# Performance work log

Hardware: AMD Instinct MI355X
Metric: run time of the kernel (lower is better)

Reference implementation:

```python
import jax, jax.numpy as jnp
import numpy as np

B, F = 65536, 300
SIGMA = 2.0
ALPHA = 1.0


def _gaussian_kernel(sigma):
    l = int(np.round(3 * sigma + 1.0))  # 7 for sigma=2
    x = np.linspace(-(l - 1.0) / 2.0, (l - 1.0) / 2.0, l)
    k = np.exp(-0.5 * np.square(x) / np.square(sigma))
    return (k / k.sum()).astype(np.float32)


def setup_inputs() -> dict:
    key = jax.random.key(0)
    fr_funcs = jax.random.normal(key, (B, F), dtype=jnp.float32)
    freqs = np.arange(1, F + 1, dtype=np.float32)
    freqs = (freqs - freqs.min()) / (freqs.max() - freqs.min())
    freqs = freqs * 2.0 - 1.0  # normalized to [-1, 1], as in __init__
    return {
        "fr_funcs": fr_funcs,
        "freqs": jnp.asarray(freqs),
        "kernel": jnp.asarray(_gaussian_kernel(SIGMA)),
    }


def _first_peak_loss(f, freqs):
    # Replicates softlocalmax's first segment.
    # find_peaks on symmetric-padded signal => boundary is a peak iff it
    # strictly exceeds its single neighbor; interior peaks are strict local maxima.
    n = f.shape[0]
    interior = (f[1:-1] > f[:-2]) & (f[1:-1] > f[2:])
    is_peak = jnp.concatenate([f[0:1] > f[1:2], interior, f[-1:] > f[-2:-1]])
    idx = jnp.where(is_peak, jnp.arange(n, dtype=jnp.int32), n)
    two = jnp.sort(idx)[:2]  # first two peak positions (n if absent)
    npeaks = jnp.sum(is_peak.astype(jnp.int32))
    # first segment end: midpoint of first two peaks (int truncation), else n-1
    end = jnp.where(npeaks >= 2, (two[0] + two[1]) // 2, n - 1)
    mask = jnp.arange(n) < end
    logits = jnp.where(mask, f * ALPHA, -jnp.inf)
    w = jax.nn.softmax(logits)  # zeros outside segment == softmax over slice
    softargmax = w @ freqs
    return -softargmax


def reference(fr_funcs, freqs, kernel):
    # Gaussian1DBlur: conv1d with padding='same' (zero padding, odd kernel)
    blurred = jax.lax.conv_general_dilated(
        fr_funcs[:, None, :], kernel[None, None, :], (1,), "SAME"
    )[:, 0]  # (B, F)
    return jax.vmap(_first_peak_loss, in_axes=(0, None))(blurred, freqs)
```

## Files before the change

### kernel.cpp

```cpp
#include <hip/hip_runtime.h>
#include <math.h>

#define NF 300
#define NC 75
#define ROWS 32
#define G 8
#define CPL 10

#define CONV(b0,b1,b2,b3,c0,c1,c2,A,B) \
    b0 = kk[0]*c0;  b0=fmaf(kk[1],c1 ,b0); b0=fmaf(kk[2],c2 ,b0); b0=fmaf(kk[3],A.x,b0); b0=fmaf(kk[4],A.y,b0); b0=fmaf(kk[5],A.z,b0); b0=fmaf(kk[6],A.w,b0); \
    b1 = kk[0]*c1;  b1=fmaf(kk[1],c2 ,b1); b1=fmaf(kk[2],A.x,b1); b1=fmaf(kk[3],A.y,b1); b1=fmaf(kk[4],A.z,b1); b1=fmaf(kk[5],A.w,b1); b1=fmaf(kk[6],B.x,b1); \
    b2 = kk[0]*c2;  b2=fmaf(kk[1],A.x,b2); b2=fmaf(kk[2],A.y,b2); b2=fmaf(kk[3],A.z,b2); b2=fmaf(kk[4],A.w,b2); b2=fmaf(kk[5],B.x,b2); b2=fmaf(kk[6],B.y,b2); \
    b3 = kk[0]*A.x; b3=fmaf(kk[1],A.y,b3); b3=fmaf(kk[2],A.z,b3); b3=fmaf(kk[3],A.w,b3); b3=fmaf(kk[4],B.x,b3); b3=fmaf(kk[5],B.y,b3); b3=fmaf(kk[6],B.z,b3);

__global__ __launch_bounds__(256) void peak_mover_loss_kernel(
    const float* __restrict__ in,
    const float* __restrict__ freqs,
    const float* __restrict__ kw,
    float* __restrict__ out)
{
    __shared__ __align__(16) float lds[ROWS * NF];

    const int tid = threadIdx.x;
    const int rowBase = blockIdx.x * ROWS;

    {
        const float4* gin = reinterpret_cast<const float4*>(in + (size_t)rowBase * NF);
        float4* l4 = reinterpret_cast<float4*>(lds);
#pragma unroll
        for (int i = 0; i < 10; ++i) {
            const int idx = tid + 256 * i;
            if (idx < ROWS * NC) l4[idx] = gin[idx];
        }
    }

    float kk[7];
#pragma unroll
    for (int t = 0; t < 7; ++t) kk[t] = kw[t];

    __syncthreads();

    const int g = tid >> 3;
    const int l = tid & 7;
    const float4* rp4 = reinterpret_cast<const float4*>(lds + g * NF);

    const int cs = CPL * l;
    const int nc = (l == G - 1) ? (NC - cs) : CPL;

    float c0, c1, c2, prev1, prev2;
    if (l == 0) {
        c0 = c1 = c2 = 0.f; prev1 = prev2 = -INFINITY;
    } else {
        const float4 P = rp4[cs - 2];
        const float4 Q = rp4[cs - 1];
        const float4 Rv = rp4[cs];
        float pb0, pb1, pb2, pb3;
        float pc0 = P.y, pc1 = P.z, pc2 = P.w;
        CONV(pb0, pb1, pb2, pb3, pc0, pc1, pc2, Q, Rv);
        (void)pb0; (void)pb1;
        prev2 = pb2; prev1 = pb3;
        c0 = Q.y; c1 = Q.z; c2 = Q.w;
    }

    int cnt = 0, p0 = 0, p1 = 0;
    float4 A = rp4[cs];
    for (int t = 0; t < nc; ++t) {
        const int m = cs + t;
        float4 B = make_float4(0.f, 0.f, 0.f, 0.f);
        if (m + 1 < NC) B = rp4[m + 1];
        float b0, b1, b2, b3;
        CONV(b0, b1, b2, b3, c0, c1, c2, A, B);
        const int base = 4 * m;
        if (prev1 > prev2 && prev1 > b0) { if (cnt==0) p0=base-1; else if (cnt==1) p1=base-1; ++cnt; }
        if (b0 > prev1 && b0 > b1)       { if (cnt==0) p0=base;   else if (cnt==1) p1=base;   ++cnt; }
        if (b1 > b0 && b1 > b2)          { if (cnt==0) p0=base+1; else if (cnt==1) p1=base+1; ++cnt; }
        if (b2 > b1 && b2 > b3)          { if (cnt==0) p0=base+2; else if (cnt==1) p1=base+2; ++cnt; }
        prev2 = b2; prev1 = b3;
        c0 = A.y; c1 = A.z; c2 = A.w;
        A = B;
    }
    if (l == G - 1 && prev1 > prev2) { if (cnt==0) p0=NF-1; else if (cnt==1) p1=NF-1; ++cnt; }

#pragma unroll
    for (int o = 1; o < G; o <<= 1) {
        const int oc = __shfl_xor(cnt, o, G);
        const int q0 = __shfl_xor(p0, o, G);
        const int q1 = __shfl_xor(p1, o, G);
        const bool right = (l & o) != 0;
        const int Lc = right ? oc : cnt, Rc = right ? cnt : oc;
        const int L0 = right ? q0 : p0,  R0 = right ? p0 : q0;
        const int L1 = right ? q1 : p1,  R1 = right ? p1 : q1;
        p0 = (Lc >= 1) ? L0 : R0;
        p1 = (Lc >= 2) ? L1 : ((Lc == 1) ? R0 : R1);
        cnt = min(Lc + Rc, 2);
    }
    const int end = (cnt >= 2) ? ((p0 + p1) >> 1) : (NF - 1);

    const float fsc = 2.0f / 299.0f;
    float s = 0.f, tt = 0.f;
    if (4 * cs < end) {
        float d0, d1, d2;
        if (l == 0) { d0 = d1 = d2 = 0.f; }
        else { const float4 Q = rp4[cs - 1]; d0 = Q.y; d1 = Q.z; d2 = Q.w; }
        float4 A2 = rp4[cs];
        for (int t = 0; t < nc; ++t) {
            const int m = cs + t;
            const int base = 4 * m;
            if (base >= end) break;
            float4 B = make_float4(0.f, 0.f, 0.f, 0.f);
            if (m + 1 < NC) B = rp4[m + 1];
            float b0, b1, b2, b3;
            CONV(b0, b1, b2, b3, d0, d1, d2, A2, B);
            if (base     < end) { float e=__expf(b0); s+=e; tt=fmaf(e, fmaf((float)(base  ), fsc, -1.f), tt); }
            if (base + 1 < end) { float e=__expf(b1); s+=e; tt=fmaf(e, fmaf((float)(base+1), fsc, -1.f), tt); }
            if (base + 2 < end) { float e=__expf(b2); s+=e; tt=fmaf(e, fmaf((float)(base+2), fsc, -1.f), tt); }
            if (base + 3 < end) { float e=__expf(b3); s+=e; tt=fmaf(e, fmaf((float)(base+3), fsc, -1.f), tt); }
            d0 = A2.y; d1 = A2.z; d2 = A2.w;
            A2 = B;
        }
    }
#pragma unroll
    for (int o = 1; o < G; o <<= 1) {
        s  += __shfl_xor(s,  o, G);
        tt += __shfl_xor(tt, o, G);
    }
    if (l == 0) out[rowBase + g] = -(tt / s);
}

extern "C" void kernel_launch(void* const* d_in, const int* in_sizes, int n_in,
                              void* d_out, int out_size, void* d_ws, size_t ws_size,
                              hipStream_t stream) {
    const float* fr    = (const float*)d_in[0];
    const float* freqs = (const float*)d_in[1];
    const float* kw    = (const float*)d_in[2];
    float* outp = (float*)d_out;

    const int nrows = in_sizes[0] / NF;
    const int block = 256;
    const int grid  = nrows / ROWS;
    peak_mover_loss_kernel<<<grid, block, 0, stream>>>(fr, freqs, kw, outp);
}
```

Measured before the change: 123.1 us.

## Scan rows in windows from global memory with early exit after two peaks

Drops the LDS staging of whole rows. Each row is now handled by 4 lanes that read directly from global memory in windows of 20 float4 chunks, and the scan stops once two peaks are found. If both peaks fall in the first window, the blurred values kept in registers are reused for the softmax. Otherwise the needed prefix is reloaded and re-convolved. The aim is to avoid reading and convolving the full row when peaks appear early. The cost is smaller, less coalesced global reads per lane and more divergent control flow.

After: 114.6 us. -6.9%, faster.

```diff
diff --git a/kernel.cpp b/kernel.cpp
--- a/kernel.cpp
+++ b/kernel.cpp
@@ -3,9 +3,10 @@
 
 #define NF 300
 #define NC 75
-#define ROWS 32
-#define G 8
-#define CPL 10
+#define G 4
+#define CPW 5
+#define WCH (G*CPW)
+#define NW 4
 
 #define CONV(b0,b1,b2,b3,c0,c1,c2,A,B) \
     b0 = kk[0]*c0;  b0=fmaf(kk[1],c1 ,b0); b0=fmaf(kk[2],c2 ,b0); b0=fmaf(kk[3],A.x,b0); b0=fmaf(kk[4],A.y,b0); b0=fmaf(kk[5],A.z,b0); b0=fmaf(kk[6],A.w,b0); \
@@ -19,112 +20,138 @@
     const float* __restrict__ kw,
     float* __restrict__ out)
 {
-    __shared__ __align__(16) float lds[ROWS * NF];
-
     const int tid = threadIdx.x;
-    const int rowBase = blockIdx.x * ROWS;
-
-    {
-        const float4* gin = reinterpret_cast<const float4*>(in + (size_t)rowBase * NF);
-        float4* l4 = reinterpret_cast<float4*>(lds);
-#pragma unroll
-        for (int i = 0; i < 10; ++i) {
-            const int idx = tid + 256 * i;
-            if (idx < ROWS * NC) l4[idx] = gin[idx];
-        }
-    }
+    const int l   = tid & (G - 1);
+    const int row = blockIdx.x * (256 / G) + (tid >> 2);
+    const float4* rp4 = reinterpret_cast<const float4*>(in + (size_t)row * NF);
 
     float kk[7];
 #pragma unroll
     for (int t = 0; t < 7; ++t) kk[t] = kw[t];
 
-    __syncthreads();
+    float bl[CPW][4];
+    int Cnt = 0, P0 = 0, P1 = 0;
+    int wexit = NW;
 
-    const int g = tid >> 3;
-    const int l = tid & 7;
-    const float4* rp4 = reinterpret_cast<const float4*>(lds + g * NF);
+#pragma unroll 1
+    for (int w = 0; w < NW; ++w) {
+        const int cs = WCH * w + CPW * l;
+        const int nc = (cs < NC) ? ((NC - cs < CPW) ? (NC - cs) : CPW) : 0;
+        int cnt = 0, p0 = 0, p1 = 0;
 
-    const int cs = CPL * l;
-    const int nc = (l == G - 1) ? (NC - cs) : CPL;
+        if (nc > 0) {
+            float4 ch[CPW + 1];
+#pragma unroll
+            for (int t = 0; t <= CPW; ++t) {
+                float4 v = make_float4(0.f, 0.f, 0.f, 0.f);
+                if (t <= nc && cs + t < NC) v = rp4[cs + t];
+                ch[t] = v;
+            }
 
-    float c0, c1, c2, prev1, prev2;
-    if (l == 0) {
-        c0 = c1 = c2 = 0.f; prev1 = prev2 = -INFINITY;
-    } else {
-        const float4 P = rp4[cs - 2];
-        const float4 Q = rp4[cs - 1];
-        const float4 Rv = rp4[cs];
-        float pb0, pb1, pb2, pb3;
-        float pc0 = P.y, pc1 = P.z, pc2 = P.w;
-        CONV(pb0, pb1, pb2, pb3, pc0, pc1, pc2, Q, Rv);
-        (void)pb0; (void)pb1;
-        prev2 = pb2; prev1 = pb3;
-        c0 = Q.y; c1 = Q.z; c2 = Q.w;
+            float c0, c1, c2, prev1, prev2;
+            if (cs == 0) {
+                c0 = c1 = c2 = 0.f; prev1 = prev2 = -INFINITY;
+            } else {
+                const float4 P = rp4[cs - 2];
+                const float4 Q = rp4[cs - 1];
+                float pb0, pb1, pb2, pb3;
+                float pc0 = P.y, pc1 = P.z, pc2 = P.w;
+                CONV(pb0, pb1, pb2, pb3, pc0, pc1, pc2, Q, ch[0]);
+                (void)pb0; (void)pb1;
+                prev2 = pb2; prev1 = pb3;
+                c0 = Q.y; c1 = Q.z; c2 = Q.w;
+            }
+
+#pragma unroll
+            for (int t = 0; t < CPW; ++t) {
+                if (t < nc) {
+                    float b0, b1, b2, b3;
+                    CONV(b0, b1, b2, b3, c0, c1, c2, ch[t], ch[t + 1]);
+                    bl[t][0] = b0; bl[t][1] = b1; bl[t][2] = b2; bl[t][3] = b3;
+                    const int base = 4 * (cs + t);
+                    if (prev1 > prev2 && prev1 > b0) { if (cnt==0) p0=base-1; else if (cnt==1) p1=base-1; ++cnt; }
+                    if (b0 > prev1 && b0 > b1)       { if (cnt==0) p0=base;   else if (cnt==1) p1=base;   ++cnt; }
+                    if (b1 > b0 && b1 > b2)          { if (cnt==0) p0=base+1; else if (cnt==1) p1=base+1; ++cnt; }
+                    if (b2 > b1 && b2 > b3)          { if (cnt==0) p0=base+2; else if (cnt==1) p1=base+2; ++cnt; }
+                    prev2 = b2; prev1 = b3;
+                    c0 = ch[t].y; c1 = ch[t].z; c2 = ch[t].w;
+                }
+            }
+            if (cs + nc == NC && prev1 > prev2) { if (cnt==0) p0=NF-1; else if (cnt==1) p1=NF-1; ++cnt; }
+        }
+
+#pragma unroll
+        for (int o = 1; o < G; o <<= 1) {
+            const int oc = __shfl_xor(cnt, o, G);
+            const int q0 = __shfl_xor(p0, o, G);
+            const int q1 = __shfl_xor(p1, o, G);
+            const bool right = (l & o) != 0;
+            const int Lc = right ? oc : cnt, Rc = right ? cnt : oc;
+            const int L0 = right ? q0 : p0,  R0 = right ? p0 : q0;
+            const int L1 = right ? q1 : p1,  R1 = right ? p1 : q1;
+            p0 = (Lc >= 1) ? L0 : R0;
+            p1 = (Lc >= 2) ? L1 : ((Lc == 1) ? R0 : R1);
+            cnt = (Lc + Rc < 2) ? (Lc + Rc) : 2;
+        }
+        if (Cnt == 0)      { P0 = p0; P1 = p1; Cnt = cnt; }
+        else if (Cnt == 1) { if (cnt >= 1) { P1 = p0; Cnt = 2; } }
+        if (Cnt >= 2) { wexit = w; break; }
     }
 
-    int cnt = 0, p0 = 0, p1 = 0;
-    float4 A = rp4[cs];
-    for (int t = 0; t < nc; ++t) {
-        const int m = cs + t;
-        float4 B = make_float4(0.f, 0.f, 0.f, 0.f);
-        if (m + 1 < NC) B = rp4[m + 1];
-        float b0, b1, b2, b3;
-        CONV(b0, b1, b2, b3, c0, c1, c2, A, B);
-        const int base = 4 * m;
-        if (prev1 > prev2 && prev1 > b0) { if (cnt==0) p0=base-1; else if (cnt==1) p1=base-1; ++cnt; }
-        if (b0 > prev1 && b0 > b1)       { if (cnt==0) p0=base;   else if (cnt==1) p1=base;   ++cnt; }
-        if (b1 > b0 && b1 > b2)          { if (cnt==0) p0=base+1; else if (cnt==1) p1=base+1; ++cnt; }
-        if (b2 > b1 && b2 > b3)          { if (cnt==0) p0=base+2; else if (cnt==1) p1=base+2; ++cnt; }
-        prev2 = b2; prev1 = b3;
-        c0 = A.y; c1 = A.z; c2 = A.w;
-        A = B;
-    }
-    if (l == G - 1 && prev1 > prev2) { if (cnt==0) p0=NF-1; else if (cnt==1) p1=NF-1; ++cnt; }
-
-#pragma unroll
-    for (int o = 1; o < G; o <<= 1) {
-        const int oc = __shfl_xor(cnt, o, G);
-        const int q0 = __shfl_xor(p0, o, G);
-        const int q1 = __shfl_xor(p1, o, G);
-        const bool right = (l & o) != 0;
-        const int Lc = right ? oc : cnt, Rc = right ? cnt : oc;
-        const int L0 = right ? q0 : p0,  R0 = right ? p0 : q0;
-        const int L1 = right ? q1 : p1,  R1 = right ? p1 : q1;
-        p0 = (Lc >= 1) ? L0 : R0;
-        p1 = (Lc >= 2) ? L1 : ((Lc == 1) ? R0 : R1);
-        cnt = min(Lc + Rc, 2);
-    }
-    const int end = (cnt >= 2) ? ((p0 + p1) >> 1) : (NF - 1);
+    const int end = (Cnt >= 2) ? ((P0 + P1) >> 1) : (NF - 1);
 
     const float fsc = 2.0f / 299.0f;
     float s = 0.f, tt = 0.f;
-    if (4 * cs < end) {
-        float d0, d1, d2;
-        if (l == 0) { d0 = d1 = d2 = 0.f; }
-        else { const float4 Q = rp4[cs - 1]; d0 = Q.y; d1 = Q.z; d2 = Q.w; }
-        float4 A2 = rp4[cs];
-        for (int t = 0; t < nc; ++t) {
-            const int m = cs + t;
-            const int base = 4 * m;
-            if (base >= end) break;
-            float4 B = make_float4(0.f, 0.f, 0.f, 0.f);
-            if (m + 1 < NC) B = rp4[m + 1];
-            float b0, b1, b2, b3;
-            CONV(b0, b1, b2, b3, d0, d1, d2, A2, B);
-            if (base     < end) { float e=__expf(b0); s+=e; tt=fmaf(e, fmaf((float)(base  ), fsc, -1.f), tt); }
-            if (base + 1 < end) { float e=__expf(b1); s+=e; tt=fmaf(e, fmaf((float)(base+1), fsc, -1.f), tt); }
-            if (base + 2 < end) { float e=__expf(b2); s+=e; tt=fmaf(e, fmaf((float)(base+2), fsc, -1.f), tt); }
-            if (base + 3 < end) { float e=__expf(b3); s+=e; tt=fmaf(e, fmaf((float)(base+3), fsc, -1.f), tt); }
-            d0 = A2.y; d1 = A2.z; d2 = A2.w;
-            A2 = B;
+
+    if (wexit == 0) {
+        const int jb = 4 * CPW * l;
+#pragma unroll
+        for (int t = 0; t < CPW; ++t) {
+#pragma unroll
+            for (int e = 0; e < 4; ++e) {
+                const int j = jb + 4 * t + e;
+                if (j < end) {
+                    const float ev = __expf(bl[t][e]);
+                    s += ev;
+                    tt = fmaf(ev, fmaf((float)j, fsc, -1.f), tt);
+                }
+            }
+        }
+    } else {
+#pragma unroll 1
+        for (int w2 = 0; w2 * (4 * WCH) < end; ++w2) {
+            const int cs2 = WCH * w2 + CPW * l;
+            if (cs2 < NC && 4 * cs2 < end) {
+                float d0, d1, d2;
+                if (cs2 == 0) { d0 = d1 = d2 = 0.f; }
+                else { const float4 Q = rp4[cs2 - 1]; d0 = Q.y; d1 = Q.z; d2 = Q.w; }
+                float4 A2 = rp4[cs2];
+#pragma unroll 1
+                for (int t = 0; t < CPW; ++t) {
+                    const int m = cs2 + t;
+                    const int base = 4 * m;
+                    if (m >= NC || base >= end) break;
+                    float4 Bv = make_float4(0.f, 0.f, 0.f, 0.f);
+                    if (m + 1 < NC) Bv = rp4[m + 1];
+                    float b0, b1, b2, b3;
+                    CONV(b0, b1, b2, b3, d0, d1, d2, A2, Bv);
+                    if (base     < end) { float e=__expf(b0); s+=e; tt=fmaf(e, fmaf((float)(base  ), fsc, -1.f), tt); }
+                    if (base + 1 < end) { float e=__expf(b1); s+=e; tt=fmaf(e, fmaf((float)(base+1), fsc, -1.f), tt); }
+                    if (base + 2 < end) { float e=__expf(b2); s+=e; tt=fmaf(e, fmaf((float)(base+2), fsc, -1.f), tt); }
+                    if (base + 3 < end) { float e=__expf(b3); s+=e; tt=fmaf(e, fmaf((float)(base+3), fsc, -1.f), tt); }
+                    d0 = A2.y; d1 = A2.z; d2 = A2.w;
+                    A2 = Bv;
+                }
+            }
         }
     }
+
 #pragma unroll
     for (int o = 1; o < G; o <<= 1) {
         s  += __shfl_xor(s,  o, G);
         tt += __shfl_xor(tt, o, G);
     }
-    if (l == 0) out[rowBase + g] = -(tt / s);
+    if (l == 0) out[row] = -(tt / s);
 }
 
 extern "C" void kernel_launch(void* const* d_in, const int* in_sizes, int n_in,
@@ -137,6 +164,6 @@
 
     const int nrows = in_sizes[0] / NF;
     const int block = 256;
-    const int grid  = nrows / ROWS;
+    const int grid  = (nrows * G) / block;
     peak_mover_loss_kernel<<<grid, block, 0, stream>>>(fr, freqs, kw, outp);
 }
```
